# Kernel optimization log

Measured on AMD Instinct MI355X. Metric: run time of the kernel, lower is better.

## Reference

```python
import jax, jax.numpy as jnp
import numpy as np

N = 100000      # nodes
E = 1280000     # random edges (self-loops added in reference, as PyG GATConv does)
F_IN = 12
HID = 64
HEADS = 4
G = 64          # graphs in batch
EPS_BN = 1e-5


def setup_inputs() -> dict:
    key = jax.random.key(0)
    ks = jax.random.split(key, 32)
    nrm = lambda k, s: jax.random.normal(k, s, jnp.float32) * 0.1
    inp = {
        "x": jax.random.normal(ks[0], (N, F_IN), jnp.float32),
        "edge_index": jax.random.randint(ks[1], (2, E), 0, N),
        "batch": jnp.sort(jax.random.randint(ks[2], (N,), 0, G)),
        # GATConv layer 1: in 12 -> 4 heads x 16, concat -> 64
        "W1": nrm(ks[3], (F_IN, HID)), "as1": nrm(ks[4], (HEADS, HID // HEADS)),
        "ad1": nrm(ks[5], (HEADS, HID // HEADS)), "b1": jnp.zeros((HID,), jnp.float32),
        "g1": jnp.ones((HID,), jnp.float32), "be1": jnp.zeros((HID,), jnp.float32),
        "W2": nrm(ks[6], (HID, HID)), "as2": nrm(ks[7], (HEADS, HID // HEADS)),
        "ad2": nrm(ks[8], (HEADS, HID // HEADS)), "b2": jnp.zeros((HID,), jnp.float32),
        "g2": jnp.ones((HID,), jnp.float32), "be2": jnp.zeros((HID,), jnp.float32),
        # GATConv layer 3: 64 -> 1 head x 64, concat=False (mean over 1 head)
        "W3": nrm(ks[9], (HID, HID)), "as3": nrm(ks[10], (1, HID)),
        "ad3": nrm(ks[11], (1, HID)), "b3": jnp.zeros((HID,), jnp.float32),
        "g3": jnp.ones((HID,), jnp.float32), "be3": jnp.zeros((HID,), jnp.float32),
        # classifier 64 -> 32 -> 2
        "Wc1": nrm(ks[12], (HID, HID // 2)), "bc1": jnp.zeros((HID // 2,), jnp.float32),
        "Wc2": nrm(ks[13], (HID // 2, 2)), "bc2": jnp.zeros((2,), jnp.float32),
        # embedding head 64 -> 64
        "We": nrm(ks[14], (HID, HID)), "bee": jnp.zeros((HID,), jnp.float32),
    }
    return inp


def _gat_layer(x, src, dst, W, a_src, a_dst, b, heads, concat):
    n = x.shape[0]
    c = W.shape[1] // heads
    h = (x @ W).reshape(n, heads, c)                      # [N,H,C]
    al_s = jnp.einsum('nhc,hc->nh', h, a_src)             # source term
    al_d = jnp.einsum('nhc,hc->nh', h, a_dst)             # target term
    e = jax.nn.leaky_relu(al_s[src] + al_d[dst], 0.2)     # [E,H]
    # segment softmax over incoming edges of each target node
    m = jax.ops.segment_max(e, dst, num_segments=n)
    ex = jnp.exp(e - m[dst])
    s = jax.ops.segment_sum(ex, dst, num_segments=n)
    alpha = ex / (s[dst] + 1e-16)                          # [E,H]
    msg = h[src] * alpha[:, :, None]                       # [E,H,C]
    out = jax.ops.segment_sum(msg, dst, num_segments=n)    # [N,H,C]
    out = out.reshape(n, heads * c) if concat else out.mean(axis=1)
    return out + b


def _bn(x, g, be):
    mu = x.mean(axis=0)
    var = x.var(axis=0)
    return (x - mu) * jax.lax.rsqrt(var + EPS_BN) * g + be


def reference(x, edge_index, batch,
              W1, as1, ad1, b1, g1, be1,
              W2, as2, ad2, b2, g2, be2,
              W3, as3, ad3, b3, g3, be3,
              Wc1, bc1, Wc2, bc2, We, bee):
    n = x.shape[0]
    loops = jnp.arange(n)
    src = jnp.concatenate([edge_index[0], loops])   # add self-loops (PyG default)
    dst = jnp.concatenate([edge_index[1], loops])

    h = _gat_layer(x, src, dst, W1, as1, ad1, b1, HEADS, True)
    h = jax.nn.elu(_bn(h, g1, be1))
    h = _gat_layer(h, src, dst, W2, as2, ad2, b2, HEADS, True)
    h = jax.nn.elu(_bn(h, g2, be2))
    h = _gat_layer(h, src, dst, W3, as3, ad3, b3, 1, False)
    h = jax.nn.elu(_bn(h, g3, be3))
    node_embeddings = h

    # global mean pool per graph
    sums = jax.ops.segment_sum(h, batch, num_segments=G)
    cnts = jax.ops.segment_sum(jnp.ones((n, 1), h.dtype), batch, num_segments=G)
    graph_emb = sums / jnp.maximum(cnts, 1.0)

    logits = jax.nn.relu(graph_emb @ Wc1 + bc1) @ Wc2 + bc2
    embedding = graph_emb @ We + bee
    return (logits, embedding, node_embeddings)
```

## Files before the change

kernel.cpp:

```cpp
#include <hip/hip_runtime.h>
#include <hip/hip_bf16.h>
#include <math.h>

#define THREADS 256
#define NBUCK 64
#define EPB 4096
#define RSB_SHIFT 8

__device__ __forceinline__ float lrelu02(float x) { return x >= 0.f ? x : 0.2f * x; }
__device__ __forceinline__ float b2f(__hip_bfloat16 v) { return __bfloat162float(v); }
__device__ __forceinline__ short f2bf_bits(float v) {
  __hip_bfloat16 hb = __float2bfloat16(v);
  return *reinterpret_cast<short*>(&hb);
}

using bf16x8 = __attribute__((ext_vector_type(8))) short;
using f32x4  = __attribute__((ext_vector_type(4))) float;

__global__ void prep_k(const float* __restrict__ W2, const float* __restrict__ W3,
                       __hip_bfloat16* __restrict__ wt2, __hip_bfloat16* __restrict__ wt3,
                       int N, int E, int* __restrict__ offs, float* __restrict__ statsRep,
                       float* __restrict__ poolbuf, float* __restrict__ padA,
                       float* __restrict__ padB) {
  int tid = blockIdx.x * THREADS + threadIdx.x;
  int stride = gridDim.x * THREADS;
  if (tid == 0) offs[N] = E;
  for (int i = tid; i < 3 * NBUCK * 128; i += stride) statsRep[i] = 0.f;
  for (int i = tid; i < 4096; i += stride) {
    poolbuf[i] = 0.f;
    padA[i] = 0.f;
    padB[i] = 0.f;
  }
  for (int i = tid; i < 4096; i += stride) {
    int n = i >> 6, k = i & 63;
    wt2[n * 64 + k] = __float2bfloat16(W2[k * 64 + n]);
    wt3[n * 64 + k] = __float2bfloat16(W3[k * 64 + n]);
  }
}

__global__ void count_tf1_k(const int* __restrict__ dstv, int* __restrict__ gcnt,
                            int E, int NBLK, int nbkt,
                            const float* __restrict__ x, const float* __restrict__ W1,
                            const float* __restrict__ aS, const float* __restrict__ aD,
                            __hip_bfloat16* __restrict__ h, float* __restrict__ als,
                            float* __restrict__ ald, int N) {
  __shared__ int cnt[512];
  __shared__ float xs[4][12];
  int tid = threadIdx.x;
  if ((int)blockIdx.x < NBLK) {
    for (int i = tid; i < nbkt; i += THREADS) cnt[i] = 0;
    __syncthreads();
    int e0 = blockIdx.x * EPB;
    int e1 = e0 + EPB; if (e1 > E) e1 = E;
    for (int i = e0 + tid; i < e1; i += THREADS)
      atomicAdd(&cnt[__builtin_nontemporal_load(dstv + i) >> RSB_SHIFT], 1);
    __syncthreads();
    for (int i = tid; i < nbkt; i += THREADS)
      gcnt[(long long)i * NBLK + blockIdx.x] = cnt[i];
    return;
  }
  int wave = tid >> 6, lane = tid & 63;
  int n = (blockIdx.x - NBLK) * 4 + wave;
  if (n < N && lane < 12) xs[wave][lane] = x[(long long)n * 12 + lane];
  __syncthreads();
  if (n >= N) return;
  float acc = 0.f;
#pragma unroll
  for (int k = 0; k < 12; k++) acc += xs[wave][k] * W1[k * 64 + lane];
  h[(long long)n * 64 + lane] = __float2bfloat16(acc);
  float ts = acc * aS[lane], td = acc * aD[lane];
  for (int m = 1; m < 16; m <<= 1) {
    ts += __shfl_xor(ts, m, 64);
    td += __shfl_xor(td, m, 64);
  }
  if ((lane & 15) == 0) {
    int hh = lane >> 4;
    als[(long long)n * 4 + hh] = ts;
    ald[(long long)n * 4 + hh] = td;
  }
}

__global__ void scan1_k(const int* __restrict__ in, int* __restrict__ out,
                        int* __restrict__ bsums, int L) {
  __shared__ int s[THREADS];
  int i = blockIdx.x * THREADS + threadIdx.x;
  int v = (i < L) ? in[i] : 0;
  s[threadIdx.x] = v;
  __syncthreads();
  for (int off = 1; off < THREADS; off <<= 1) {
    int t = (threadIdx.x >= off) ? s[threadIdx.x - off] : 0;
    __syncthreads();
    s[threadIdx.x] += t;
    __syncthreads();
  }
  if (i < L) out[i] = s[threadIdx.x] - v;
  if (threadIdx.x == THREADS - 1) bsums[blockIdx.x] = s[THREADS - 1];
}

__global__ void scan2_k(int* bsums, int nb) {
  __shared__ int s[1024];
  int tid = threadIdx.x;
  int v = (tid < nb) ? bsums[tid] : 0;
  s[tid] = v;
  __syncthreads();
  for (int off = 1; off < 1024; off <<= 1) {
    int t = (tid >= off) ? s[tid - off] : 0;
    __syncthreads();
    s[tid] += t;
    __syncthreads();
  }
  if (tid < nb) bsums[tid] = s[tid] - v;
}

__global__ void scan3b_k(int* __restrict__ a, const int* __restrict__ bsums, int L) {
  int i = blockIdx.x * THREADS + threadIdx.x;
  if (i < L) a[i] += bsums[blockIdx.x];
}

__global__ void binscatter_k(const int* __restrict__ srcv, const int* __restrict__ dstv,
                             const int* __restrict__ gbase, int2* __restrict__ binned,
                             int E, int NBLK, int nbkt) {
  __shared__ int cur[512];
  int tid = threadIdx.x;
  int blk = blockIdx.x;
  for (int i = tid; i < nbkt; i += THREADS) cur[i] = gbase[(long long)i * NBLK + blk];
  __syncthreads();
  int e0 = blk * EPB;
  int e1 = e0 + EPB; if (e1 > E) e1 = E;
  for (int i = e0 + tid; i < e1; i += THREADS) {
    int d = __builtin_nontemporal_load(dstv + i);
    int s = __builtin_nontemporal_load(srcv + i);
    int p = atomicAdd(&cur[d >> RSB_SHIFT], 1);
    binned[p] = make_int2(s, d);
  }
}

__global__ void bucket_csr_k(const int2* __restrict__ binned, const int* __restrict__ gbase,
                             int* __restrict__ offs, int* __restrict__ csr,
                             int N, int E, int NBLK, int nbkt) {
  __shared__ int lcnt[256];
  __shared__ int lofs[256];
  int b = blockIdx.x;
  int lo = b << RSB_SHIFT;
  int tid = threadIdx.x;
  int b0 = gbase[(long long)b * NBLK];
  int b1 = (b + 1 < nbkt) ? gbase[(long long)(b + 1) * NBLK] : E;
  lcnt[tid] = 0;
  __syncthreads();
  for (int i = b0 + tid; i < b1; i += THREADS)
    atomicAdd(&lcnt[binned[i].y - lo], 1);
  __syncthreads();
  int v = lcnt[tid];
  lofs[tid] = v;
  __syncthreads();
  for (int off = 1; off < 256; off <<= 1) {
    int t = (tid >= off) ? lofs[tid - off] : 0;
    __syncthreads();
    lofs[tid] += t;
    __syncthreads();
  }
  int excl = lofs[tid] - v;
  int node = lo + tid;
  if (node < N) offs[node] = b0 + excl;
  lcnt[tid] = excl;
  __syncthreads();
  for (int i = b0 + tid; i < b1; i += THREADS) {
    int2 e = binned[i];
    int r = atomicAdd(&lcnt[e.y - lo], 1);
    csr[b0 + r] = e.x;
  }
}

__device__ __forceinline__ void compute_ssc(const float* __restrict__ rep,
                                            const float* __restrict__ g,
                                            const float* __restrict__ be,
                                            float* sscS, int N) {
  int tid = threadIdx.x;
  if (tid < 128) {
    float a = 0.f;
#pragma unroll 8
    for (int b = 0; b < NBUCK; b++) a += rep[b * 128 + tid];
    sscS[tid] = a;
  }
  __syncthreads();
  if (tid < 64) {
    float inv = 1.f / (float)N;
    float mu = sscS[tid] * inv;
    float var = sscS[64 + tid] * inv - mu * mu;
    float sc = rsqrtf(var + 1e-5f) * g[tid];
    sscS[tid] = sc;
    sscS[64 + tid] = be[tid] - mu * sc;
  }
  __syncthreads();
}

template <int H>
__global__ __launch_bounds__(256) void transform_mfma(
    const float* __restrict__ pre, const float* __restrict__ statsRep,
    const float* __restrict__ g0, const float* __restrict__ be0,
    const __hip_bfloat16* __restrict__ wt,
    const float* __restrict__ aS, const float* __restrict__ aD,
    __hip_bfloat16* __restrict__ h, float* __restrict__ als, float* __restrict__ ald,
    int N) {
  __shared__ float sscS[128];
  compute_ssc(statsRep, g0, be0, sscS, N);
  int wid = threadIdx.x >> 6, lane = threadIdx.x & 63;
  int m0 = blockIdx.x * 64 + wid * 16;
  int r = lane & 15, g = lane >> 4;
  const float* arow = pre + (long long)(m0 + r) * 64;
  int k0 = g * 8;
  bf16x8 a0, a1;
#pragma unroll
  for (int i = 0; i < 8; i++) {
    int ka = k0 + i, kb = k0 + 32 + i;
    float va = arow[ka] * sscS[ka] + sscS[64 + ka];
    float vb = arow[kb] * sscS[kb] + sscS[64 + kb];
    va = va > 0.f ? va : (__expf(va) - 1.f);
    vb = vb > 0.f ? vb : (__expf(vb) - 1.f);
    a0[i] = f2bf_bits(va);
    a1[i] = f2bf_bits(vb);
  }
  f32x4 acc[4];
#pragma unroll
  for (int s = 0; s < 4; s++) acc[s] = (f32x4){0.f, 0.f, 0.f, 0.f};
#pragma unroll
  for (int s = 0; s < 4; s++) {
    const bf16x8* brow = (const bf16x8*)(wt + (s * 16 + r) * 64 + k0);
    acc[s] = __builtin_amdgcn_mfma_f32_16x16x32_bf16(a0, brow[0], acc[s], 0, 0, 0);
    acc[s] = __builtin_amdgcn_mfma_f32_16x16x32_bf16(a1, brow[4], acc[s], 0, 0, 0);
  }
  float asum[4] = {0.f, 0.f, 0.f, 0.f}, dsum[4] = {0.f, 0.f, 0.f, 0.f};
#pragma unroll
  for (int s = 0; s < 4; s++) {
    int n = s * 16 + r;
    float sv = aS[n], dv = aD[n];
    float ts[4], td[4];
#pragma unroll
    for (int j = 0; j < 4; j++) { ts[j] = acc[s][j] * sv; td[j] = acc[s][j] * dv; }
#pragma unroll
    for (int mk = 1; mk < 16; mk <<= 1) {
#pragma unroll
      for (int j = 0; j < 4; j++) {
        ts[j] += __shfl_xor(ts[j], mk, 64);
        td[j] += __shfl_xor(td[j], mk, 64);
      }
    }
#pragma unroll
    for (int j = 0; j < 4; j++) {
      int m = m0 + g * 4 + j;
      if (m < N) {
        h[(long long)m * 64 + n] = __float2bfloat16(acc[s][j]);
        if (H == 4) {
          if (r == 0) { als[m * 4 + s] = ts[j]; ald[m * 4 + s] = td[j]; }
        }
      }
      if (H == 1) { asum[j] += ts[j]; dsum[j] += td[j]; }
    }
  }
  if (H == 1 && r == 0) {
#pragma unroll
    for (int j = 0; j < 4; j++) {
      int m = m0 + g * 4 + j;
      if (m < N) { als[m] = asum[j]; ald[m] = dsum[j]; }
    }
  }
}

__global__ void gat_gather4(const __hip_bfloat16* __restrict__ h, const float* __restrict__ als,
                            const float* __restrict__ ald, const int* __restrict__ offs,
                            const int* __restrict__ csr, const float* __restrict__ bias,
                            float* __restrict__ pre, float* __restrict__ statsRep, int N) {
  int wid = threadIdx.x >> 6, lane = threadIdx.x & 63;
  int n = blockIdx.x * 4 + wid;
  bool active = n < N;
  int t = lane & 3;
  int e = lane >> 2;
  int hh = lane >> 4;
  __shared__ float red[4][128];

  float v = 0.f;
  if (active) {
    float aldt = ald[n * 4 + t];
    float exs = __expf(lrelu02(als[n * 4 + t] + aldt));
    float sacc = 0.f;
    float acc = 0.f;
    int e0 = offs[n], e1 = offs[n + 1];

    for (int t0 = e0; t0 < e1; t0 += 16) {
      int idx = t0 + e;
      bool act = idx < e1;
      int sn = act ? csr[idx] : 0;
      float ex = act ? __expf(lrelu02(als[sn * 4 + t] + aldt)) : 0.f;
      sacc += ex;
#pragma unroll
      for (int j = 0; j < 16; j++) {
        int sj = __builtin_amdgcn_readlane(sn, j << 2);
        float exj = __shfl(ex, (j << 2) + hh, 64);
        acc += b2f(h[(long long)sj * 64 + lane]) * exj;
      }
    }
#pragma unroll
    for (int ms = 4; ms < 64; ms <<= 1) sacc += __shfl_xor(sacc, ms, 64);
    float s = sacc + exs;
    float exsb = __shfl(exs, hh, 64);
    float sb = __shfl(s, hh, 64);
    acc += b2f(h[(long long)n * 64 + lane]) * exsb;
    v = acc / (sb + 1e-16f) + bias[lane];
    pre[(long long)n * 64 + lane] = v;
  }
  red[wid][lane] = v;
  red[wid][64 + lane] = v * v;
  __syncthreads();
  if (threadIdx.x < 128) {
    float s4 = red[0][threadIdx.x] + red[1][threadIdx.x] + red[2][threadIdx.x] + red[3][threadIdx.x];
    atomicAdd(&statsRep[(blockIdx.x & (NBUCK - 1)) * 128 + threadIdx.x], s4);
  }
}

__global__ void gat_gather1(const __hip_bfloat16* __restrict__ h, const float* __restrict__ als,
                            const float* __restrict__ ald, const int* __restrict__ offs,
                            const int* __restrict__ csr, const float* __restrict__ bias,
                            float* __restrict__ pre, float* __restrict__ statsRep, int N) {
  int wid = threadIdx.x >> 6, lane = threadIdx.x & 63;
  int n = blockIdx.x * 4 + wid;
  bool active = n < N;
  __shared__ float red[4][128];

  float v = 0.f;
  if (active) {
    float aldn = ald[n];
    float exs = __expf(lrelu02(als[n] + aldn));
    float sacc = 0.f, acc = 0.f;
    int e0 = offs[n], e1 = offs[n + 1];

    for (int t0 = e0; t0 < e1; t0 += 64) {
      int idx = t0 + lane;
      bool act = idx < e1;
      int sn = act ? csr[idx] : 0;
      float ex = act ? __expf(lrelu02(als[sn] + aldn)) : 0.f;
      sacc += ex;
      int cnt = e1 - t0;
#pragma unroll
      for (int c = 0; c < 4; c++) {
        if (c * 16 >= cnt) break;
#pragma unroll
        for (int j = 0; j < 16; j++) {
          int ln = c * 16 + j;
          int sj = __builtin_amdgcn_readlane(sn, ln);
          float exj = __int_as_float(__builtin_amdgcn_readlane(__float_as_int(ex), ln));
          acc += b2f(h[(long long)sj * 64 + lane]) * exj;
        }
      }
    }
#pragma unroll
    for (int ms = 1; ms < 64; ms <<= 1) sacc += __shfl_xor(sacc, ms, 64);
    float s = sacc + exs;
    acc += b2f(h[(long long)n * 64 + lane]) * exs;
    v = acc / (s + 1e-16f) + bias[lane];
    pre[(long long)n * 64 + lane] = v;
  }
  red[wid][lane] = v;
  red[wid][64 + lane] = v * v;
  __syncthreads();
  if (threadIdx.x < 128) {
    float s4 = red[0][threadIdx.x] + red[1][threadIdx.x] + red[2][threadIdx.x] + red[3][threadIdx.x];
    atomicAdd(&statsRep[(blockIdx.x & (NBUCK - 1)) * 128 + threadIdx.x], s4);
  }
}

__global__ void emb_pool_k(const float* __restrict__ pre, const float* __restrict__ statsRep,
                           const float* __restrict__ g0, const float* __restrict__ be0,
                           const int* __restrict__ batch, float* __restrict__ nemb,
                           float* __restrict__ pool, int N, int per) {
  __shared__ float sscS[128];
  compute_ssc(statsRep, g0, be0, sscS, N);
  int lane = threadIdx.x & 63, wid = threadIdx.x >> 6;
  int gw = blockIdx.x * 4 + wid;
  int n0 = gw * per;
  int n1 = n0 + per; if (n1 > N) n1 = N;
  if (n0 >= n1) return;
  float sc = sscS[lane], sh = sscS[64 + lane];
  float acc = 0.f;
  int cg = batch[n0];
  for (int n = n0; n < n1; n++) {
    int g = batch[n];
    if (g != cg) { atomicAdd(&pool[cg * 64 + lane], acc); acc = 0.f; cg = g; }
    float v = pre[(long long)n * 64 + lane] * sc + sh;
    v = v > 0.f ? v : (__expf(v) - 1.f);
    nemb[(long long)n * 64 + lane] = v;
    acc += v;
  }
  atomicAdd(&pool[cg * 64 + lane], acc);
}

__global__ void head_k(const float* __restrict__ pool, const int* __restrict__ batch,
                       const float* __restrict__ Wc1, const float* __restrict__ bc1,
                       const float* __restrict__ Wc2, const float* __restrict__ bc2,
                       const float* __restrict__ We, const float* __restrict__ bee,
                       float* __restrict__ logits, float* __restrict__ emb, int N) {
  int g = blockIdx.x, lane = threadIdx.x;
  __shared__ float pr[64], hid[32];
  __shared__ int bnds[2];
  if (lane < 2) {
    int target = g + lane;
    int lo = 0, hi = N;
    while (lo < hi) {
      int mid = (lo + hi) >> 1;
      if (batch[mid] < target) lo = mid + 1; else hi = mid;
    }
    bnds[lane] = lo;
  }
  __syncthreads();
  float cnt = (float)(bnds[1] - bnds[0]);
  pr[lane] = pool[g * 64 + lane] / fmaxf(cnt, 1.f);
  __syncthreads();
  if (lane < 32) {
    float a = bc1[lane];
    for (int k = 0; k < 64; k++) a += pr[k] * Wc1[k * 32 + lane];
    hid[lane] = fmaxf(a, 0.f);
  }
  float e = bee[lane];
  for (int k = 0; k < 64; k++) e += pr[k] * We[k * 64 + lane];
  emb[g * 64 + lane] = e;
  __syncthreads();
  if (lane < 2) {
    float l = bc2[lane];
    for (int k = 0; k < 32; k++) l += hid[k] * Wc2[k * 2 + lane];
    logits[g * 2 + lane] = l;
  }
}

extern "C" void kernel_launch(void* const* d_in, const int* in_sizes, int n_in,
                              void* d_out, int out_size, void* d_ws, size_t ws_size,
                              hipStream_t stream) {
  const float* x    = (const float*)d_in[0];
  const int*   ei   = (const int*)d_in[1];
  const int*   batch= (const int*)d_in[2];
  const float* W1   = (const float*)d_in[3];
  const float* as1  = (const float*)d_in[4];
  const float* ad1  = (const float*)d_in[5];
  const float* b1   = (const float*)d_in[6];
  const float* g1   = (const float*)d_in[7];
  const float* be1  = (const float*)d_in[8];
  const float* W2   = (const float*)d_in[9];
  const float* as2  = (const float*)d_in[10];
  const float* ad2  = (const float*)d_in[11];
  const float* b2   = (const float*)d_in[12];
  const float* g2   = (const float*)d_in[13];
  const float* be2  = (const float*)d_in[14];
  const float* W3   = (const float*)d_in[15];
  const float* as3  = (const float*)d_in[16];
  const float* ad3  = (const float*)d_in[17];
  const float* b3   = (const float*)d_in[18];
  const float* g3   = (const float*)d_in[19];
  const float* be3  = (const float*)d_in[20];
  const float* Wc1  = (const float*)d_in[21];
  const float* bc1  = (const float*)d_in[22];
  const float* Wc2  = (const float*)d_in[23];
  const float* bc2  = (const float*)d_in[24];
  const float* We   = (const float*)d_in[25];
  const float* bee  = (const float*)d_in[26];

  int N = in_sizes[0] / 12;
  int E = in_sizes[1] / 2;
  const int* srcv = ei;
  const int* dstv = ei + E;

  char* p = (char*)d_ws;
  auto carve = [&](size_t bytes) -> char* {
    char* r = p;
    p += (bytes + 255) & ~(size_t)255;
    return r;
  };
  int NBLK = (E + EPB - 1) / EPB;
  int nbkt = (N + 255) >> RSB_SHIFT;
  long long L = (long long)nbkt * NBLK;

  int* offs    = (int*)carve((size_t)(N + 1) * 4);
  int* gcnt    = (int*)carve((size_t)L * 4);
  int* gbase   = (int*)carve((size_t)L * 4);
  int* bsums   = (int*)carve(4096 * 4);
  int* csr     = (int*)carve((size_t)E * 4);
  int2* binned = (int2*)carve((size_t)E * 8);
  __hip_bfloat16* h  = (__hip_bfloat16*)carve((size_t)N * 64 * 2);
  __hip_bfloat16* wt2 = (__hip_bfloat16*)carve(64 * 64 * 2);
  __hip_bfloat16* wt3 = (__hip_bfloat16*)carve(64 * 64 * 2);
  float* als   = (float*)carve((size_t)N * 4 * 4);
  float* ald   = (float*)carve((size_t)N * 4 * 4);
  float* preA  = (float*)carve((size_t)(N + 64) * 64 * 4);
  float* preB  = (float*)carve((size_t)(N + 64) * 64 * 4);
  float* statsRep = (float*)carve(3 * NBUCK * 128 * 4);
  float* poolbuf  = (float*)carve(64 * 64 * 4);

  int nbNode = (N + 3) / 4;
  int nbT = (N + 63) / 64;
  int nbL = (int)((L + THREADS - 1) / THREADS);

  prep_k<<<128, THREADS, 0, stream>>>(W2, W3, wt2, wt3, N, E, offs, statsRep,
                                      poolbuf, preA + (size_t)N * 64, preB + (size_t)N * 64);
  count_tf1_k<<<NBLK + nbNode, THREADS, 0, stream>>>(dstv, gcnt, E, NBLK, nbkt,
                                                     x, W1, as1, ad1, h, als, ald, N);
  scan1_k<<<nbL, THREADS, 0, stream>>>(gcnt, gbase, bsums, (int)L);
  scan2_k<<<1, 1024, 0, stream>>>(bsums, nbL);
  scan3b_k<<<nbL, THREADS, 0, stream>>>(gbase, bsums, (int)L);
  binscatter_k<<<NBLK, THREADS, 0, stream>>>(srcv, dstv, gbase, binned, E, NBLK, nbkt);
  bucket_csr_k<<<nbkt, THREADS, 0, stream>>>(binned, gbase, offs, csr, N, E, NBLK, nbkt);

  gat_gather4<<<nbNode, THREADS, 0, stream>>>(h, als, ald, offs, csr, b1, preA, statsRep, N);
  transform_mfma<4><<<nbT, THREADS, 0, stream>>>(preA, statsRep, g1, be1, wt2, as2, ad2, h, als, ald, N);
  gat_gather4<<<nbNode, THREADS, 0, stream>>>(h, als, ald, offs, csr, b2, preB, statsRep + NBUCK * 128, N);
  transform_mfma<1><<<nbT, THREADS, 0, stream>>>(preB, statsRep + NBUCK * 128, g2, be2, wt3, as3, ad3, h, als, ald, N);
  gat_gather1<<<nbNode, THREADS, 0, stream>>>(h, als, ald, offs, csr, b3, preA, statsRep + 2 * NBUCK * 128, N);

  float* outF   = (float*)d_out;
  float* logits = outF;
  float* emb    = outF + 64 * 2;
  float* nemb   = outF + 64 * 2 + 64 * 64;

  const int PER = 16;
  int nWaves = (N + PER - 1) / PER;
  int nbPool = (nWaves + 3) / 4;
  emb_pool_k<<<nbPool, THREADS, 0, stream>>>(preA, statsRep + 2 * NBUCK * 128, g3, be3,
                                             batch, nemb, poolbuf, N, PER);
  head_k<<<64, 64, 0, stream>>>(poolbuf, batch, Wc1, bc1, Wc2, bc2, We, bee, logits, emb, N);
}
```

Before: 299.9 us.

## Fuse CSR build stages into one cooperative kernel and pack binned edges

Merges the prep kernel into the count/transform launch as extra blocks. Replaces the three scan kernels, binscatter and bucket CSR kernels with a single cooperative kernel that uses grid-wide syncs between phases. Packs each binned edge into one 32-bit word (source shifted left by 8, low byte local destination) instead of an int2, which halves that buffer's traffic. This cuts launch gaps at the cost of grid.sync overhead, and the packing assumes source indices fit in 24 bits.

```diff
diff --git a/kernel.cpp b/kernel.cpp
--- a/kernel.cpp
+++ b/kernel.cpp
@@ -1,6 +1,9 @@
 #include <hip/hip_runtime.h>
 #include <hip/hip_bf16.h>
+#include <hip/hip_cooperative_groups.h>
 #include <math.h>
+
+namespace cg = cooperative_groups;
 
 #define THREADS 256
 #define NBUCK 64
@@ -17,33 +20,17 @@
 using bf16x8 = __attribute__((ext_vector_type(8))) short;
 using f32x4  = __attribute__((ext_vector_type(4))) float;
 
-__global__ void prep_k(const float* __restrict__ W2, const float* __restrict__ W3,
-                       __hip_bfloat16* __restrict__ wt2, __hip_bfloat16* __restrict__ wt3,
-                       int N, int E, int* __restrict__ offs, float* __restrict__ statsRep,
-                       float* __restrict__ poolbuf, float* __restrict__ padA,
-                       float* __restrict__ padB) {
-  int tid = blockIdx.x * THREADS + threadIdx.x;
-  int stride = gridDim.x * THREADS;
-  if (tid == 0) offs[N] = E;
-  for (int i = tid; i < 3 * NBUCK * 128; i += stride) statsRep[i] = 0.f;
-  for (int i = tid; i < 4096; i += stride) {
-    poolbuf[i] = 0.f;
-    padA[i] = 0.f;
-    padB[i] = 0.f;
-  }
-  for (int i = tid; i < 4096; i += stride) {
-    int n = i >> 6, k = i & 63;
-    wt2[n * 64 + k] = __float2bfloat16(W2[k * 64 + n]);
-    wt3[n * 64 + k] = __float2bfloat16(W3[k * 64 + n]);
-  }
-}
-
 __global__ void count_tf1_k(const int* __restrict__ dstv, int* __restrict__ gcnt,
                             int E, int NBLK, int nbkt,
                             const float* __restrict__ x, const float* __restrict__ W1,
                             const float* __restrict__ aS, const float* __restrict__ aD,
                             __hip_bfloat16* __restrict__ h, float* __restrict__ als,
-                            float* __restrict__ ald, int N) {
+                            float* __restrict__ ald, int N, int nbNode,
+                            const float* __restrict__ W2, const float* __restrict__ W3,
+                            __hip_bfloat16* __restrict__ wt2, __hip_bfloat16* __restrict__ wt3,
+                            int* __restrict__ offs, float* __restrict__ statsRep,
+                            float* __restrict__ poolbuf, float* __restrict__ padA,
+                            float* __restrict__ padB) {
   __shared__ int cnt[512];
   __shared__ float xs[4][12];
   int tid = threadIdx.x;
@@ -59,115 +46,135 @@
       gcnt[(long long)i * NBLK + blockIdx.x] = cnt[i];
     return;
   }
-  int wave = tid >> 6, lane = tid & 63;
-  int n = (blockIdx.x - NBLK) * 4 + wave;
-  if (n < N && lane < 12) xs[wave][lane] = x[(long long)n * 12 + lane];
-  __syncthreads();
-  if (n >= N) return;
-  float acc = 0.f;
-#pragma unroll
-  for (int k = 0; k < 12; k++) acc += xs[wave][k] * W1[k * 64 + lane];
-  h[(long long)n * 64 + lane] = __float2bfloat16(acc);
-  float ts = acc * aS[lane], td = acc * aD[lane];
-  for (int m = 1; m < 16; m <<= 1) {
-    ts += __shfl_xor(ts, m, 64);
-    td += __shfl_xor(td, m, 64);
-  }
-  if ((lane & 15) == 0) {
-    int hh = lane >> 4;
-    als[(long long)n * 4 + hh] = ts;
-    ald[(long long)n * 4 + hh] = td;
-  }
-}
-
-__global__ void scan1_k(const int* __restrict__ in, int* __restrict__ out,
-                        int* __restrict__ bsums, int L) {
-  __shared__ int s[THREADS];
-  int i = blockIdx.x * THREADS + threadIdx.x;
-  int v = (i < L) ? in[i] : 0;
-  s[threadIdx.x] = v;
-  __syncthreads();
-  for (int off = 1; off < THREADS; off <<= 1) {
-    int t = (threadIdx.x >= off) ? s[threadIdx.x - off] : 0;
-    __syncthreads();
-    s[threadIdx.x] += t;
-    __syncthreads();
-  }
-  if (i < L) out[i] = s[threadIdx.x] - v;
-  if (threadIdx.x == THREADS - 1) bsums[blockIdx.x] = s[THREADS - 1];
-}
-
-__global__ void scan2_k(int* bsums, int nb) {
-  __shared__ int s[1024];
-  int tid = threadIdx.x;
-  int v = (tid < nb) ? bsums[tid] : 0;
-  s[tid] = v;
-  __syncthreads();
-  for (int off = 1; off < 1024; off <<= 1) {
-    int t = (tid >= off) ? s[tid - off] : 0;
-    __syncthreads();
-    s[tid] += t;
-    __syncthreads();
-  }
-  if (tid < nb) bsums[tid] = s[tid] - v;
-}
-
-__global__ void scan3b_k(int* __restrict__ a, const int* __restrict__ bsums, int L) {
-  int i = blockIdx.x * THREADS + threadIdx.x;
-  if (i < L) a[i] += bsums[blockIdx.x];
-}
-
-__global__ void binscatter_k(const int* __restrict__ srcv, const int* __restrict__ dstv,
-                             const int* __restrict__ gbase, int2* __restrict__ binned,
-                             int E, int NBLK, int nbkt) {
-  __shared__ int cur[512];
+  if ((int)blockIdx.x < NBLK + nbNode) {
+    int wave = tid >> 6, lane = tid & 63;
+    int n = (blockIdx.x - NBLK) * 4 + wave;
+    if (n < N && lane < 12) xs[wave][lane] = x[(long long)n * 12 + lane];
+    __syncthreads();
+    if (n >= N) return;
+    float acc = 0.f;
+#pragma unroll
+    for (int k = 0; k < 12; k++) acc += xs[wave][k] * W1[k * 64 + lane];
+    h[(long long)n * 64 + lane] = __float2bfloat16(acc);
+    float ts = acc * aS[lane], td = acc * aD[lane];
+    for (int m = 1; m < 16; m <<= 1) {
+      ts += __shfl_xor(ts, m, 64);
+      td += __shfl_xor(td, m, 64);
+    }
+    if ((lane & 15) == 0) {
+      int hh = lane >> 4;
+      als[(long long)n * 4 + hh] = ts;
+      ald[(long long)n * 4 + hh] = td;
+    }
+    return;
+  }
+  int pb = blockIdx.x - NBLK - nbNode;
+  int gtid = pb * THREADS + tid;
+  int stride = 32 * THREADS;
+  if (gtid == 0) offs[N] = E;
+  for (int i = gtid; i < 3 * NBUCK * 128; i += stride) statsRep[i] = 0.f;
+  for (int i = gtid; i < 4096; i += stride) {
+    poolbuf[i] = 0.f;
+    padA[i] = 0.f;
+    padB[i] = 0.f;
+    int n = i >> 6, k = i & 63;
+    wt2[n * 64 + k] = __float2bfloat16(W2[k * 64 + n]);
+    wt3[n * 64 + k] = __float2bfloat16(W3[k * 64 + n]);
+  }
+}
+
+__global__ void csrbuild_k(const int* __restrict__ srcv, const int* __restrict__ dstv,
+                           const int* __restrict__ gcnt, int* __restrict__ gbase,
+                           int* __restrict__ bsums, unsigned int* __restrict__ binned,
+                           int* __restrict__ offs, int* __restrict__ csr,
+                           int E, int N, int NBLK, int nbkt, int L, int nbL) {
+  cg::grid_group grid = cg::this_grid();
+  __shared__ int shm[512];
   int tid = threadIdx.x;
   int blk = blockIdx.x;
-  for (int i = tid; i < nbkt; i += THREADS) cur[i] = gbase[(long long)i * NBLK + blk];
-  __syncthreads();
-  int e0 = blk * EPB;
-  int e1 = e0 + EPB; if (e1 > E) e1 = E;
-  for (int i = e0 + tid; i < e1; i += THREADS) {
-    int d = __builtin_nontemporal_load(dstv + i);
-    int s = __builtin_nontemporal_load(srcv + i);
-    int p = atomicAdd(&cur[d >> RSB_SHIFT], 1);
-    binned[p] = make_int2(s, d);
-  }
-}
-
-__global__ void bucket_csr_k(const int2* __restrict__ binned, const int* __restrict__ gbase,
-                             int* __restrict__ offs, int* __restrict__ csr,
-                             int N, int E, int NBLK, int nbkt) {
-  __shared__ int lcnt[256];
-  __shared__ int lofs[256];
-  int b = blockIdx.x;
-  int lo = b << RSB_SHIFT;
-  int tid = threadIdx.x;
-  int b0 = gbase[(long long)b * NBLK];
-  int b1 = (b + 1 < nbkt) ? gbase[(long long)(b + 1) * NBLK] : E;
-  lcnt[tid] = 0;
-  __syncthreads();
-  for (int i = b0 + tid; i < b1; i += THREADS)
-    atomicAdd(&lcnt[binned[i].y - lo], 1);
-  __syncthreads();
-  int v = lcnt[tid];
-  lofs[tid] = v;
-  __syncthreads();
-  for (int off = 1; off < 256; off <<= 1) {
-    int t = (tid >= off) ? lofs[tid - off] : 0;
-    __syncthreads();
-    lofs[tid] += t;
-    __syncthreads();
-  }
-  int excl = lofs[tid] - v;
-  int node = lo + tid;
-  if (node < N) offs[node] = b0 + excl;
-  lcnt[tid] = excl;
-  __syncthreads();
-  for (int i = b0 + tid; i < b1; i += THREADS) {
-    int2 e = binned[i];
-    int r = atomicAdd(&lcnt[e.y - lo], 1);
-    csr[b0 + r] = e.x;
+
+  if (blk < nbL) {
+    int i = blk * THREADS + tid;
+    int v = (i < L) ? gcnt[i] : 0;
+    shm[tid] = v;
+    __syncthreads();
+    for (int off = 1; off < THREADS; off <<= 1) {
+      int t = (tid >= off) ? shm[tid - off] : 0;
+      __syncthreads();
+      shm[tid] += t;
+      __syncthreads();
+    }
+    if (i < L) gbase[i] = shm[tid] - v;
+    if (tid == THREADS - 1) bsums[blk] = shm[THREADS - 1];
+  }
+  grid.sync();
+
+  if (blk == 0) {
+    int o0 = (tid < nbL) ? bsums[tid] : 0;
+    int o1 = (tid + 256 < nbL) ? bsums[tid + 256] : 0;
+    shm[tid] = o0; shm[tid + 256] = o1;
+    __syncthreads();
+    for (int off = 1; off < 512; off <<= 1) {
+      int a = (tid >= off) ? shm[tid - off] : 0;
+      int b = (tid + 256 >= off) ? shm[tid + 256 - off] : 0;
+      __syncthreads();
+      shm[tid] += a;
+      shm[tid + 256] += b;
+      __syncthreads();
+    }
+    if (tid < nbL) bsums[tid] = shm[tid] - o0;
+    if (tid + 256 < nbL) bsums[tid + 256] = shm[tid + 256] - o1;
+  }
+  grid.sync();
+
+  if (blk < nbL) {
+    int i = blk * THREADS + tid;
+    if (i < L) gbase[i] += bsums[blk];
+  }
+  grid.sync();
+
+  if (blk < NBLK) {
+    for (int i = tid; i < nbkt; i += THREADS) shm[i] = gbase[(long long)i * NBLK + blk];
+    __syncthreads();
+    int e0 = blk * EPB;
+    int e1 = e0 + EPB; if (e1 > E) e1 = E;
+    for (int i = e0 + tid; i < e1; i += THREADS) {
+      int d = __builtin_nontemporal_load(dstv + i);
+      int s = __builtin_nontemporal_load(srcv + i);
+      int p = atomicAdd(&shm[d >> RSB_SHIFT], 1);
+      binned[p] = ((unsigned)s << 8) | (unsigned)(d & 255);
+    }
+  }
+  grid.sync();
+
+  if (blk < nbkt) {
+    int lo = blk << RSB_SHIFT;
+    int b0 = gbase[(long long)blk * NBLK];
+    int b1 = (blk + 1 < nbkt) ? gbase[(long long)(blk + 1) * NBLK] : E;
+    shm[tid] = 0;
+    __syncthreads();
+    for (int i = b0 + tid; i < b1; i += THREADS)
+      atomicAdd(&shm[binned[i] & 255u], 1);
+    __syncthreads();
+    int v = shm[tid];
+    shm[256 + tid] = v;
+    __syncthreads();
+    for (int off = 1; off < 256; off <<= 1) {
+      int t = (tid >= off) ? shm[256 + tid - off] : 0;
+      __syncthreads();
+      shm[256 + tid] += t;
+      __syncthreads();
+    }
+    int excl = shm[256 + tid] - v;
+    int node = lo + tid;
+    if (node < N) offs[node] = b0 + excl;
+    shm[tid] = excl;
+    __syncthreads();
+    for (int i = b0 + tid; i < b1; i += THREADS) {
+      unsigned e = binned[i];
+      int r = atomicAdd(&shm[e & 255u], 1);
+      csr[b0 + r] = (int)(e >> 8);
+    }
   }
 }
 
@@ -381,16 +388,16 @@
   if (n0 >= n1) return;
   float sc = sscS[lane], sh = sscS[64 + lane];
   float acc = 0.f;
-  int cg = batch[n0];
+  int cg0 = batch[n0];
   for (int n = n0; n < n1; n++) {
     int g = batch[n];
-    if (g != cg) { atomicAdd(&pool[cg * 64 + lane], acc); acc = 0.f; cg = g; }
+    if (g != cg0) { atomicAdd(&pool[cg0 * 64 + lane], acc); acc = 0.f; cg0 = g; }
     float v = pre[(long long)n * 64 + lane] * sc + sh;
     v = v > 0.f ? v : (__expf(v) - 1.f);
     nemb[(long long)n * 64 + lane] = v;
     acc += v;
   }
-  atomicAdd(&pool[cg * 64 + lane], acc);
+  atomicAdd(&pool[cg0 * 64 + lane], acc);
 }
 
 __global__ void head_k(const float* __restrict__ pool, const int* __restrict__ batch,
@@ -475,13 +482,15 @@
   int NBLK = (E + EPB - 1) / EPB;
   int nbkt = (N + 255) >> RSB_SHIFT;
   long long L = (long long)nbkt * NBLK;
+  int Li = (int)L;
+  int nbL = (Li + THREADS - 1) / THREADS;
 
   int* offs    = (int*)carve((size_t)(N + 1) * 4);
   int* gcnt    = (int*)carve((size_t)L * 4);
   int* gbase   = (int*)carve((size_t)L * 4);
   int* bsums   = (int*)carve(4096 * 4);
   int* csr     = (int*)carve((size_t)E * 4);
-  int2* binned = (int2*)carve((size_t)E * 8);
+  unsigned int* binned = (unsigned int*)carve((size_t)E * 4);
   __hip_bfloat16* h  = (__hip_bfloat16*)carve((size_t)N * 64 * 2);
   __hip_bfloat16* wt2 = (__hip_bfloat16*)carve(64 * 64 * 2);
   __hip_bfloat16* wt3 = (__hip_bfloat16*)carve(64 * 64 * 2);
@@ -491,20 +500,24 @@
   float* preB  = (float*)carve((size_t)(N + 64) * 64 * 4);
   float* statsRep = (float*)carve(3 * NBUCK * 128 * 4);
   float* poolbuf  = (float*)carve(64 * 64 * 4);
+  float* padA = preA + (size_t)N * 64;
+  float* padB = preB + (size_t)N * 64;
 
   int nbNode = (N + 3) / 4;
   int nbT = (N + 63) / 64;
-  int nbL = (int)((L + THREADS - 1) / THREADS);
-
-  prep_k<<<128, THREADS, 0, stream>>>(W2, W3, wt2, wt3, N, E, offs, statsRep,
-                                      poolbuf, preA + (size_t)N * 64, preB + (size_t)N * 64);
-  count_tf1_k<<<NBLK + nbNode, THREADS, 0, stream>>>(dstv, gcnt, E, NBLK, nbkt,
-                                                     x, W1, as1, ad1, h, als, ald, N);
-  scan1_k<<<nbL, THREADS, 0, stream>>>(gcnt, gbase, bsums, (int)L);
-  scan2_k<<<1, 1024, 0, stream>>>(bsums, nbL);
-  scan3b_k<<<nbL, THREADS, 0, stream>>>(gbase, bsums, (int)L);
-  binscatter_k<<<NBLK, THREADS, 0, stream>>>(srcv, dstv, gbase, binned, E, NBLK, nbkt);
-  bucket_csr_k<<<nbkt, THREADS, 0, stream>>>(binned, gbase, offs, csr, N, E, NBLK, nbkt);
+
+  count_tf1_k<<<NBLK + nbNode + 32, THREADS, 0, stream>>>(
+      dstv, gcnt, E, NBLK, nbkt, x, W1, as1, ad1, h, als, ald, N, nbNode,
+      W2, W3, wt2, wt3, offs, statsRep, poolbuf, padA, padB);
+
+  int G = nbL;
+  if (NBLK > G) G = NBLK;
+  if (nbkt > G) G = nbkt;
+  void* cargs[] = {(void*)&srcv, (void*)&dstv, (void*)&gcnt, (void*)&gbase,
+                   (void*)&bsums, (void*)&binned, (void*)&offs, (void*)&csr,
+                   (void*)&E, (void*)&N, (void*)&NBLK, (void*)&nbkt,
+                   (void*)&Li, (void*)&nbL};
+  hipLaunchCooperativeKernel((void*)csrbuild_k, dim3(G), dim3(THREADS), cargs, 0, stream);
 
   gat_gather4<<<nbNode, THREADS, 0, stream>>>(h, als, ald, offs, csr, b1, preA, statsRep, N);
   transform_mfma<4><<<nbT, THREADS, 0, stream>>>(preA, statsRep, g1, be1, wt2, as2, ad2, h, als, ald, N);
```

After: 518.1 us. +72.7%, slower.
